# Performance work log

Measured on AMD Instinct MI355X. Metric: run time of the kernel, lower is better.

## Reference

```python
import jax, jax.numpy as jnp
import numpy as np

N, L, C = 256, 256, 8
DEPTH = 4  # truncation depth; output channels = C + C^2 + ... + C^DEPTH = 4680


def _tp(a, b):
    # tensor product of flattened signature levels: [N, A] x [N, B] -> [N, A*B]
    n = a.shape[0]
    return (a[:, :, None] * b[:, None, :]).reshape(n, -1)


def _exp_levels(v, depth):
    # exp(v) in the truncated tensor algebra: level j = v^{\otimes j} / j!
    # v: [N, C]; returns tuple of [N, C^j] for j = 1..depth
    levels = [v]
    for j in range(2, depth + 1):
        levels.append(_tp(levels[-1], v) / j)
    return tuple(levels)


def _sig_forward(path, depth):
    # signature(path, depth, stream=False, basepoint=False, inverse=False, initial=None)
    # = exp(x2-x1) (x) exp(x3-x2) (x) ... (x) exp(xL - x_{L-1})
    n, l, c = path.shape
    dx = path[:, 1:] - path[:, :-1]  # [N, L-1, C] increments
    sig0 = _exp_levels(dx[:, 0], depth)

    def step(sig, v):
        # Chen's relation: new_m = sum_{j=0}^{m} sig_{m-j} (x) e_j  (sig_0 = e_0 = 1)
        e = _exp_levels(v, depth)
        new = []
        for m in range(1, depth + 1):
            t = sig[m - 1] + e[m - 1]
            for j in range(1, m):
                t = t + _tp(sig[m - j - 1], e[j - 1])
            new.append(t)
        return tuple(new), None

    xs = jnp.moveaxis(dx[:, 1:], 1, 0)  # [L-2, N, C] -- sequential recursion over stream
    sig, _ = jax.lax.scan(jax.checkpoint(step), sig0, xs)
    return jnp.concatenate(sig, axis=-1)  # [N, C + C^2 + ... + C^depth]


def setup_inputs() -> dict:
    key = jax.random.key(0)
    path = jax.random.normal(key, (N, L, C), dtype=jnp.float32)
    return {"path": path}


def reference(path):
    return _sig_forward(path, DEPTH)
```

## Files before the change

### kernel.cpp

```cpp
#include <hip/hip_runtime.h>


constexpr int N_SAMP = 256;
constexpr int L_LEN = 256;
constexpr int C_DIM = 8;
constexpr int OUT_PER = 8 + 64 + 512 + 4096;

__global__ __launch_bounds__(256) void sig_kernel(const float* __restrict__ path,
                                                  float* __restrict__ out) {
    __shared__ float dx[(L_LEN - 1) * C_DIM];

    const int n = blockIdx.x;
    const int tid = threadIdx.x;

    const float* p = path + (size_t)n * L_LEN * C_DIM;
    if (tid < L_LEN - 1) {
        float4 a0 = *(const float4*)(p + tid * C_DIM);
        float4 a1 = *(const float4*)(p + tid * C_DIM + 4);
        float4 b0 = *(const float4*)(p + (tid + 1) * C_DIM);
        float4 b1 = *(const float4*)(p + (tid + 1) * C_DIM + 4);
        float4 d0 = make_float4(b0.x - a0.x, b0.y - a0.y, b0.z - a0.z, b0.w - a0.w);
        float4 d1 = make_float4(b1.x - a1.x, b1.y - a1.y, b1.z - a1.z, b1.w - a1.w);
        *(float4*)(&dx[tid * C_DIM]) = d0;
        *(float4*)(&dx[tid * C_DIM + 4]) = d1;
    }
    __syncthreads();

    const int i = tid >> 5;
    const int j = (tid >> 2) & 7;
    const int k0 = (tid & 3) * 2;

    float acc[16];
#pragma unroll
    for (int m = 0; m < 16; ++m) acc[m] = 0.f;
    float s3a = 0.f, s3b = 0.f, s2 = 0.f, s1 = 0.f;

    constexpr float THIRD = 1.f / 3.f;

#pragma unroll 5
    for (int t = 0; t < L_LEN - 1; ++t) {
        const float* v = &dx[t * C_DIM];
        float vv[8];
#pragma unroll
        for (int c = 0; c < 8; ++c) vv[c] = v[c];
        float vi = v[i];
        float vj = v[j];
        float2 vk = *(const float2*)(v + k0);
        float vk0 = vk.x, vk1 = vk.y;

        float c4 = fmaf(vj * THIRD, fmaf(0.25f, vi, s1), s2);
        float c3 = fmaf(vj * 0.5f, fmaf(THIRD, vi, s1), s2);
        float f0 = fmaf(c4, 0.5f * vk0, s3a);
        float f1 = fmaf(c4, 0.5f * vk1, s3b);

#pragma unroll
        for (int l = 0; l < 8; ++l) {
            acc[l] = fmaf(f0, vv[l], acc[l]);
            acc[8 + l] = fmaf(f1, vv[l], acc[8 + l]);
        }
        s3a = fmaf(c3, vk0, s3a);
        s3b = fmaf(c3, vk1, s3b);
        s2 = fmaf(fmaf(0.5f, vi, s1), vj, s2);
        s1 += vi;
    }

    float* o = out + (size_t)n * OUT_PER;
    if ((tid & 31) == 0) o[i] = s1;
    if ((tid & 3) == 0) o[8 + i * 8 + j] = s2;
    *(float2*)(o + 72 + tid * 2) = make_float2(s3a, s3b);
    float4* o4 = (float4*)(o + 584 + tid * 16);
    o4[0] = make_float4(acc[0], acc[1], acc[2], acc[3]);
    o4[1] = make_float4(acc[4], acc[5], acc[6], acc[7]);
    o4[2] = make_float4(acc[8], acc[9], acc[10], acc[11]);
    o4[3] = make_float4(acc[12], acc[13], acc[14], acc[15]);
}

extern "C" void kernel_launch(void* const* d_in, const int* in_sizes, int n_in,
                              void* d_out, int out_size, void* d_ws, size_t ws_size,
                              hipStream_t stream) {
    const float* path = (const float*)d_in[0];
    float* out = (float*)d_out;
    sig_kernel<<<N_SAMP, 256, 0, stream>>>(path, out);
}
```

Baseline: 71.35 us.

## Split path into four segments and combine signatures via Chen's relation

Each block now runs 1024 threads, with four groups of 256 each computing the signature of one quarter of the increments in parallel. The partial signatures are staged in shared memory and combined sequentially with Chen's tensor-product identity, then written out from shared memory. This shortens the serial recursion per thread by about four times. In exchange it adds about 75KB of shared memory per block, three combine passes with block-wide barriers, and lower occupancy.

```diff
diff --git a/kernel.cpp b/kernel.cpp
--- a/kernel.cpp
+++ b/kernel.cpp
@@ -5,30 +5,33 @@
 constexpr int L_LEN = 256;
 constexpr int C_DIM = 8;
 constexpr int OUT_PER = 8 + 64 + 512 + 4096;
+constexpr int NSEG = 4;
+constexpr int SIG_STRIDE = 4688;
 
-__global__ __launch_bounds__(256) void sig_kernel(const float* __restrict__ path,
-                                                  float* __restrict__ out) {
+__global__ __launch_bounds__(1024) void sig_kernel(const float* __restrict__ path,
+                                                   float* __restrict__ out) {
     __shared__ float dx[(L_LEN - 1) * C_DIM];
+    __shared__ float sig[NSEG][SIG_STRIDE];
 
     const int n = blockIdx.x;
     const int tid = threadIdx.x;
 
     const float* p = path + (size_t)n * L_LEN * C_DIM;
-    if (tid < L_LEN - 1) {
-        float4 a0 = *(const float4*)(p + tid * C_DIM);
-        float4 a1 = *(const float4*)(p + tid * C_DIM + 4);
-        float4 b0 = *(const float4*)(p + (tid + 1) * C_DIM);
-        float4 b1 = *(const float4*)(p + (tid + 1) * C_DIM + 4);
-        float4 d0 = make_float4(b0.x - a0.x, b0.y - a0.y, b0.z - a0.z, b0.w - a0.w);
-        float4 d1 = make_float4(b1.x - a1.x, b1.y - a1.y, b1.z - a1.z, b1.w - a1.w);
-        *(float4*)(&dx[tid * C_DIM]) = d0;
-        *(float4*)(&dx[tid * C_DIM + 4]) = d1;
+    if (tid < 1020) {
+        float2 a = *(const float2*)(p + tid * 2);
+        float2 b = *(const float2*)(p + tid * 2 + C_DIM);
+        *(float2*)(&dx[tid * 2]) = make_float2(b.x - a.x, b.y - a.y);
     }
     __syncthreads();
 
-    const int i = tid >> 5;
-    const int j = (tid >> 2) & 7;
-    const int k0 = (tid & 3) * 2;
+    const int seg = tid >> 8;
+    const int r = tid & 255;
+    const int i = r >> 5;
+    const int j = (r >> 2) & 7;
+    const int k0 = (r & 3) * 2;
+
+    const int t0 = seg * 64;
+    const int tcnt = (seg == 3) ? 63 : 64;
 
     float acc[16];
 #pragma unroll
@@ -37,9 +40,9 @@
 
     constexpr float THIRD = 1.f / 3.f;
 
-#pragma unroll 5
-    for (int t = 0; t < L_LEN - 1; ++t) {
-        const float* v = &dx[t * C_DIM];
+#pragma unroll 4
+    for (int t = 0; t < tcnt; ++t) {
+        const float* v = &dx[(t0 + t) * C_DIM];
         float vv[8];
 #pragma unroll
         for (int c = 0; c < 8; ++c) vv[c] = v[c];
@@ -64,15 +67,67 @@
         s1 += vi;
     }
 
+    {
+        float* sg = sig[seg];
+        if ((r & 31) == 0) sg[i] = s1;
+        if ((r & 3) == 0) sg[8 + i * 8 + j] = s2;
+        *(float2*)(&sg[72 + r * 2]) = make_float2(s3a, s3b);
+        float* s4 = sg + 584 + r * 16;
+        *(float4*)(s4) = make_float4(acc[0], acc[1], acc[2], acc[3]);
+        *(float4*)(s4 + 4) = make_float4(acc[4], acc[5], acc[6], acc[7]);
+        *(float4*)(s4 + 8) = make_float4(acc[8], acc[9], acc[10], acc[11]);
+        *(float4*)(s4 + 12) = make_float4(acc[12], acc[13], acc[14], acc[15]);
+    }
+    __syncthreads();
+
+    const int i4 = tid >> 7;
+    const int j4 = (tid >> 4) & 7;
+    const int k4 = (tid >> 1) & 7;
+    const int l0 = (tid & 1) * 4;
+    const int ijk4 = tid >> 1;
+
+    for (int b = 1; b < NSEG; ++b) {
+        const float* A = sig[0];
+        const float* B = sig[b];
+
+        float a3 = A[72 + ijk4];
+        float a2 = A[8 + i4 * 8 + j4];
+        float a1 = A[i4];
+        float c4v[4];
+#pragma unroll
+        for (int m = 0; m < 4; ++m) {
+            int l = l0 + m;
+            float t = A[584 + ijk4 * 8 + l] + B[584 + ijk4 * 8 + l];
+            t = fmaf(a3, B[l], t);
+            t = fmaf(a2, B[8 + k4 * 8 + l], t);
+            t = fmaf(a1, B[72 + j4 * 64 + k4 * 8 + l], t);
+            c4v[m] = t;
+        }
+        float n3 = 0.f, n2 = 0.f, n1 = 0.f;
+        if (tid < 512) {
+            int ii = tid >> 6, jj = (tid >> 3) & 7, kk = tid & 7;
+            n3 = A[72 + tid] + B[72 + tid];
+            n3 = fmaf(A[8 + ii * 8 + jj], B[kk], n3);
+            n3 = fmaf(A[ii], B[8 + jj * 8 + kk], n3);
+        }
+        if (tid < 64) {
+            int ii = tid >> 3, jj = tid & 7;
+            n2 = A[8 + tid] + B[8 + tid] + A[ii] * B[jj];
+        }
+        if (tid < 8) n1 = A[tid] + B[tid];
+        __syncthreads();
+
+        float* W = sig[0];
+#pragma unroll
+        for (int m = 0; m < 4; ++m) W[584 + ijk4 * 8 + l0 + m] = c4v[m];
+        if (tid < 512) W[72 + tid] = n3;
+        if (tid < 64) W[8 + tid] = n2;
+        if (tid < 8) W[tid] = n1;
+        __syncthreads();
+    }
+
     float* o = out + (size_t)n * OUT_PER;
-    if ((tid & 31) == 0) o[i] = s1;
-    if ((tid & 3) == 0) o[8 + i * 8 + j] = s2;
-    *(float2*)(o + 72 + tid * 2) = make_float2(s3a, s3b);
-    float4* o4 = (float4*)(o + 584 + tid * 16);
-    o4[0] = make_float4(acc[0], acc[1], acc[2], acc[3]);
-    o4[1] = make_float4(acc[4], acc[5], acc[6], acc[7]);
-    o4[2] = make_float4(acc[8], acc[9], acc[10], acc[11]);
-    o4[3] = make_float4(acc[12], acc[13], acc[14], acc[15]);
+    for (int idx = tid; idx < OUT_PER; idx += 1024) o[idx] = sig[0][idx];
 }
 
 extern "C" void kernel_launch(void* const* d_in, const int* in_sizes, int n_in,
@@ -80,5 +135,5 @@
                               hipStream_t stream) {
     const float* path = (const float*)d_in[0];
     float* out = (float*)d_out;
-    sig_kernel<<<N_SAMP, 256, 0, stream>>>(path, out);
+    sig_kernel<<<N_SAMP, 1024, 0, stream>>>(path, out);
 }
```

Measured after the change: 67.81 us. -5.0%, faster.

## Split stream into 8 segments and combine partial signatures with Chen's identity

Applied to the files above, without the earlier changes.

The time axis is split into 8 segments of 32 steps, each handled by 64 threads that compute a partial signature, with each thread holding a full 8x8 level-4 accumulator tile in registers. The partial signatures are then merged sequentially through shared memory using Chen's relation, and the output goes out via a strided copy from shared memory. This cuts the serial dependency chain from 255 steps to 32 plus 7 combine steps and doubles the threads per block. In exchange it needs 64+ accumulator registers per thread, about 40KB of shared memory, several block-wide barriers per merge, and the merges are serialized.

```diff
diff --git a/kernel.cpp b/kernel.cpp
--- a/kernel.cpp
+++ b/kernel.cpp
@@ -3,76 +3,148 @@
 
 constexpr int N_SAMP = 256;
 constexpr int L_LEN = 256;
-constexpr int C_DIM = 8;
-constexpr int OUT_PER = 8 + 64 + 512 + 4096;
+constexpr int OUT_PER = 4680;
+constexpr int NSEG = 8;
+constexpr int S4 = 584;
+constexpr int ROW = 68;
+constexpr int SIG_WORDS = S4 + ROW * 64;
 
-__global__ __launch_bounds__(256) void sig_kernel(const float* __restrict__ path,
+__global__ __launch_bounds__(512) void sig_kernel(const float* __restrict__ path,
                                                   float* __restrict__ out) {
-    __shared__ float dx[(L_LEN - 1) * C_DIM];
+    __shared__ __align__(16) float dx[(L_LEN - 1) * 8];
+    __shared__ __align__(16) float X[SIG_WORDS];
+    __shared__ __align__(16) float Y[SIG_WORDS];
 
     const int n = blockIdx.x;
     const int tid = threadIdx.x;
 
-    const float* p = path + (size_t)n * L_LEN * C_DIM;
-    if (tid < L_LEN - 1) {
-        float4 a0 = *(const float4*)(p + tid * C_DIM);
-        float4 a1 = *(const float4*)(p + tid * C_DIM + 4);
-        float4 b0 = *(const float4*)(p + (tid + 1) * C_DIM);
-        float4 b1 = *(const float4*)(p + (tid + 1) * C_DIM + 4);
-        float4 d0 = make_float4(b0.x - a0.x, b0.y - a0.y, b0.z - a0.z, b0.w - a0.w);
-        float4 d1 = make_float4(b1.x - a1.x, b1.y - a1.y, b1.z - a1.z, b1.w - a1.w);
-        *(float4*)(&dx[tid * C_DIM]) = d0;
-        *(float4*)(&dx[tid * C_DIM + 4]) = d1;
+    const float* p = path + (size_t)n * L_LEN * 8;
+    if (tid < 510) {
+        float4 a = *(const float4*)(p + tid * 4);
+        float4 b = *(const float4*)(p + tid * 4 + 8);
+        *(float4*)(&dx[tid * 4]) = make_float4(b.x - a.x, b.y - a.y, b.z - a.z, b.w - a.w);
     }
     __syncthreads();
 
-    const int i = tid >> 5;
-    const int j = (tid >> 2) & 7;
-    const int k0 = (tid & 3) * 2;
+    const int seg = tid >> 6;
+    const int r = tid & 63;
+    const int i = r >> 3;
+    const int j = r & 7;
+    const int t0 = seg * 32;
+    const int tcnt = (seg == 7) ? 31 : 32;
 
-    float acc[16];
+    float acc[8][8];
 #pragma unroll
-    for (int m = 0; m < 16; ++m) acc[m] = 0.f;
-    float s3a = 0.f, s3b = 0.f, s2 = 0.f, s1 = 0.f;
-
+    for (int k = 0; k < 8; ++k)
+#pragma unroll
+        for (int l = 0; l < 8; ++l) acc[k][l] = 0.f;
+    float s3[8] = {0.f, 0.f, 0.f, 0.f, 0.f, 0.f, 0.f, 0.f};
+    float s2 = 0.f, s1 = 0.f;
     constexpr float THIRD = 1.f / 3.f;
 
-#pragma unroll 5
-    for (int t = 0; t < L_LEN - 1; ++t) {
-        const float* v = &dx[t * C_DIM];
-        float vv[8];
-#pragma unroll
-        for (int c = 0; c < 8; ++c) vv[c] = v[c];
+#pragma unroll 2
+    for (int t = 0; t < tcnt; ++t) {
+        const float* v = &dx[(t0 + t) * 8];
+        float4 v0 = *(const float4*)(v);
+        float4 v1 = *(const float4*)(v + 4);
+        float vv[8] = {v0.x, v0.y, v0.z, v0.w, v1.x, v1.y, v1.z, v1.w};
         float vi = v[i];
         float vj = v[j];
-        float2 vk = *(const float2*)(v + k0);
-        float vk0 = vk.x, vk1 = vk.y;
 
         float c4 = fmaf(vj * THIRD, fmaf(0.25f, vi, s1), s2);
         float c3 = fmaf(vj * 0.5f, fmaf(THIRD, vi, s1), s2);
-        float f0 = fmaf(c4, 0.5f * vk0, s3a);
-        float f1 = fmaf(c4, 0.5f * vk1, s3b);
-
+        float c4h = 0.5f * c4;
 #pragma unroll
-        for (int l = 0; l < 8; ++l) {
-            acc[l] = fmaf(f0, vv[l], acc[l]);
-            acc[8 + l] = fmaf(f1, vv[l], acc[8 + l]);
+        for (int k = 0; k < 8; ++k) {
+            float f = fmaf(c4h, vv[k], s3[k]);
+#pragma unroll
+            for (int l = 0; l < 8; ++l) acc[k][l] = fmaf(f, vv[l], acc[k][l]);
+            s3[k] = fmaf(c3, vv[k], s3[k]);
         }
-        s3a = fmaf(c3, vk0, s3a);
-        s3b = fmaf(c3, vk1, s3b);
         s2 = fmaf(fmaf(0.5f, vi, s1), vj, s2);
         s1 += vi;
     }
 
+    auto write_sig = [&](float* sg) {
+        if (j == 0) sg[i] = s1;
+        sg[8 + r] = s2;
+        *(float4*)(&sg[72 + 8 * r]) = make_float4(s3[0], s3[1], s3[2], s3[3]);
+        *(float4*)(&sg[72 + 8 * r + 4]) = make_float4(s3[4], s3[5], s3[6], s3[7]);
+        float* rowp = sg + S4 + ROW * r;
+#pragma unroll
+        for (int k = 0; k < 8; ++k) {
+            *(float4*)(rowp + 8 * k) = make_float4(acc[k][0], acc[k][1], acc[k][2], acc[k][3]);
+            *(float4*)(rowp + 8 * k + 4) = make_float4(acc[k][4], acc[k][5], acc[k][6], acc[k][7]);
+        }
+    };
+
+    if (seg == 0) write_sig(X);
+    __syncthreads();
+
+    float c4r[8];
+    {
+        const float* q = X + S4 + ROW * r + 8 * seg;
+        float4 c0 = *(const float4*)(q);
+        float4 c1 = *(const float4*)(q + 4);
+        c4r[0] = c0.x; c4r[1] = c0.y; c4r[2] = c0.z; c4r[3] = c0.w;
+        c4r[4] = c1.x; c4r[5] = c1.y; c4r[6] = c1.z; c4r[7] = c1.w;
+    }
+
+    for (int b = 1; b < NSEG; ++b) {
+        if (seg == b) write_sig(Y);
+        __syncthreads();
+
+        float4 ya = *(const float4*)(Y);
+        float4 yb = *(const float4*)(Y + 4);
+        float y1[8] = {ya.x, ya.y, ya.z, ya.w, yb.x, yb.y, yb.z, yb.w};
+        const float* y2p = Y + 8 + 8 * seg;
+        float4 u0 = *(const float4*)(y2p);
+        float4 u1 = *(const float4*)(y2p + 4);
+        float y2k[8] = {u0.x, u0.y, u0.z, u0.w, u1.x, u1.y, u1.z, u1.w};
+        const float* y3p = Y + 72 + 64 * j + 8 * seg;
+        float4 w0 = *(const float4*)(y3p);
+        float4 w1 = *(const float4*)(y3p + 4);
+        float y3[8] = {w0.x, w0.y, w0.z, w0.w, w1.x, w1.y, w1.z, w1.w};
+        const float* y4p = Y + S4 + ROW * r + 8 * seg;
+        float4 z0 = *(const float4*)(y4p);
+        float4 z1 = *(const float4*)(y4p + 4);
+        float y4[8] = {z0.x, z0.y, z0.z, z0.w, z1.x, z1.y, z1.z, z1.w};
+        float x3o = X[72 + 8 * r + seg];
+        float x2o = X[8 + r];
+        float x1o = X[i];
+
+        float n3 = X[72 + tid] + Y[72 + tid];
+        n3 = fmaf(X[8 + (tid >> 3)], Y[tid & 7], n3);
+        n3 = fmaf(X[tid >> 6], Y[8 + (tid & 63)], n3);
+        float n2 = 0.f, n1 = 0.f;
+        if (tid < 64) n2 = X[8 + tid] + Y[8 + tid] + X[tid >> 3] * Y[tid & 7];
+        if (tid < 8) n1 = X[tid] + Y[tid];
+
+#pragma unroll
+        for (int l = 0; l < 8; ++l) {
+            float t = c4r[l] + y4[l];
+            t = fmaf(x3o, y1[l], t);
+            t = fmaf(x2o, y2k[l], t);
+            t = fmaf(x1o, y3[l], t);
+            c4r[l] = t;
+        }
+
+        __syncthreads();
+        X[72 + tid] = n3;
+        if (tid < 64) X[8 + tid] = n2;
+        if (tid < 8) X[tid] = n1;
+    }
+
+    {
+        float* q = Y + S4 + 64 * r + 8 * seg;
+        *(float4*)(q) = make_float4(c4r[0], c4r[1], c4r[2], c4r[3]);
+        *(float4*)(q + 4) = make_float4(c4r[4], c4r[5], c4r[6], c4r[7]);
+    }
+    __syncthreads();
     float* o = out + (size_t)n * OUT_PER;
-    if ((tid & 31) == 0) o[i] = s1;
-    if ((tid & 3) == 0) o[8 + i * 8 + j] = s2;
-    *(float2*)(o + 72 + tid * 2) = make_float2(s3a, s3b);
-    float4* o4 = (float4*)(o + 584 + tid * 16);
-    o4[0] = make_float4(acc[0], acc[1], acc[2], acc[3]);
-    o4[1] = make_float4(acc[4], acc[5], acc[6], acc[7]);
-    o4[2] = make_float4(acc[8], acc[9], acc[10], acc[11]);
-    o4[3] = make_float4(acc[12], acc[13], acc[14], acc[15]);
+    for (int idx = tid; idx < OUT_PER; idx += 512) {
+        o[idx] = (idx < S4) ? X[idx] : Y[idx];
+    }
 }
 
 extern "C" void kernel_launch(void* const* d_in, const int* in_sizes, int n_in,
@@ -80,5 +152,5 @@
                               hipStream_t stream) {
     const float* path = (const float*)d_in[0];
     float* out = (float*)d_out;
-    sig_kernel<<<N_SAMP, 256, 0, stream>>>(path, out);
+    sig_kernel<<<N_SAMP, 512, 0, stream>>>(path, out);
 }
```

New measurement: 69.05 us. 3.2% less time.
